# Kernel optimization log

Hardware: AMD Instinct MI355X
Metric: run time of the kernel (lower is better)

## Reference

```python
import jax, jax.numpy as jnp
import numpy as np

B, S, K, N = 2, 4096, 4096, 4096
BLOCKSIZE = 128  # GPTQ group size


def _unpack_rows(q):
    # int32 [K//8, N] -> int32 [K, N], 8 nibbles packed along dim 0 (little-endian)
    shifts = (jnp.arange(8, dtype=jnp.int32) * 4)
    nib = (q[:, None, :] >> shifts[None, :, None]) & 0xF  # [K//8, 8, N]
    return nib.reshape(q.shape[0] * 8, q.shape[1])


def _unpack_cols(q):
    # int32 [G, N//8] -> int32 [G, N], 8 nibbles packed along dim 1
    shifts = (jnp.arange(8, dtype=jnp.int32) * 4)
    nib = (q[:, :, None] >> shifts[None, None, :]) & 0xF  # [G, N//8, 8]
    return nib.reshape(q.shape[0], q.shape[1] * 8)


def _dequant(qweight, scales, qzeros, blocksize):
    # GPTQ int4 dequant: w[k, n] = (q[k, n] - z[g, n]) * s[g, n], g = k // blocksize
    w_int = _unpack_rows(qweight).astype(jnp.float32)          # [K, N]
    zeros = _unpack_cols(qzeros).astype(jnp.float32)           # [G, N]
    z = jnp.repeat(zeros, blocksize, axis=0)                   # [K, N]
    s = jnp.repeat(scales, blocksize, axis=0)                  # [K, N]
    return (w_int - z) * s


def setup_inputs() -> dict:
    key = jax.random.key(0)
    ks = jax.random.split(key, 6)
    inp = jax.random.normal(ks[0], (B, S, K), dtype=jnp.float32)
    residual = jax.random.normal(ks[1], (B, S, N), dtype=jnp.float32)
    qweight = jax.random.randint(ks[2], (K // 8, N), 0, 2147483647, dtype=jnp.int32)
    qzeros = jax.random.randint(ks[3], (K // BLOCKSIZE, N // 8), 0, 2147483647, dtype=jnp.int32)
    scales = jax.random.uniform(ks[4], (K // BLOCKSIZE, N), dtype=jnp.float32, minval=1e-3, maxval=1e-2)
    bias = jax.random.normal(ks[5], (N,), dtype=jnp.float32)
    return {"input": inp, "residual": residual, "qweight": qweight,
            "scales": scales, "qzeros": qzeros, "bias": bias}


def reference(input, residual, qweight, scales, qzeros, bias):
    # Fused: dequant(int4 GPTQ) -> GEMM -> +bias -> +residual (mm_bias_add_int4)
    w = _dequant(qweight, scales, qzeros, BLOCKSIZE)           # [K, N]
    out = jnp.einsum('bsk,kn->bsn', input, w) + bias + residual
    return out
```

## Files before the change

### kernel.cpp

```cpp
#include <hip/hip_runtime.h>
#include <hip/hip_bf16.h>
#include <stdint.h>

using bf16 = __hip_bfloat16;
typedef __attribute__((ext_vector_type(8))) short short8;
typedef __attribute__((ext_vector_type(4))) float floatx4;

#define DEVINL __device__ __forceinline__

constexpr int K_DIM = 4096;
constexpr int N_DIM = 4096;
constexpr int M_DIM = 8192;

DEVINL void gload_lds16(const void* g, void* l) {
  __builtin_amdgcn_global_load_lds((const __attribute__((address_space(1))) void*)g,
                                   (__attribute__((address_space(3))) void*)l,
                                   16, 0, 0);
}

__global__ __launch_bounds__(256) void k_prep(const int* __restrict__ qw,
                                              const float* __restrict__ scales,
                                              const int* __restrict__ qz,
                                              bf16* __restrict__ wt,
                                              const float* __restrict__ a,
                                              bf16* __restrict__ ao) {
  if (blockIdx.x < 64 * 128) {
    __shared__ __align__(16) uint4 lds[32 * 8];
    const int b = blockIdx.x;
    const int kp0 = (b & 63) * 8;
    const int n0  = (b >> 6) * 32;
    const int t = threadIdx.x;
    const int n_l = t & 31, kp_l = t >> 5;
    const int n = n0 + n_l, kp = kp0 + kp_l;

    int q = qw[kp * N_DIM + n];
    int g = kp0 >> 4;
    float s = scales[g * N_DIM + n];
    int zword = qz[g * (N_DIM / 8) + (n >> 3)];
    float z = (float)((zword >> ((n & 7) * 4)) & 0xF);
    float nzs = -z * s;
    bf16 h[8];
#pragma unroll
    for (int i = 0; i < 8; ++i) {
      float w = fmaf((float)((q >> (4 * i)) & 0xF), s, nzs);
      h[i] = __float2bfloat16(w);
    }
    lds[n_l * 8 + (kp_l ^ (n_l & 7))] = *(const uint4*)h;
    __syncthreads();
    const int n_o = t >> 3, kp_o = t & 7;
    uint4 v = lds[n_o * 8 + (kp_o ^ (n_o & 7))];
    ((uint4*)wt)[(size_t)(n0 + n_o) * (K_DIM / 8) + kp0 + kp_o] = v;
  } else {
    int t = (blockIdx.x - 64 * 128) * 256 + threadIdx.x;
    const float4* a4 = (const float4*)a;
    float4 v0 = a4[2 * t], v1 = a4[2 * t + 1];
    bf16 h[8];
    h[0] = __float2bfloat16(v0.x); h[1] = __float2bfloat16(v0.y);
    h[2] = __float2bfloat16(v0.z); h[3] = __float2bfloat16(v0.w);
    h[4] = __float2bfloat16(v1.x); h[5] = __float2bfloat16(v1.y);
    h[6] = __float2bfloat16(v1.z); h[7] = __float2bfloat16(v1.w);
    ((uint4*)ao)[t] = *(const uint4*)h;
  }
}

constexpr int BM = 128, BN = 128, BK = 64;
constexpr int NBLK_N = N_DIM / BN;
constexpr int NBLK_M = M_DIM / BM;

template <bool A_IS_BF16>
__global__ __launch_bounds__(256, 2) void k_gemm(const void* __restrict__ a_ptr,
                                                 const bf16* __restrict__ wt,
                                                 const float* __restrict__ bias,
                                                 const float* __restrict__ residual,
                                                 float* __restrict__ out) {
  __shared__ __align__(16) bf16 As[BM * BK];
  __shared__ __align__(16) bf16 Bs[BN * BK];

  const int tid  = threadIdx.x;
  const int lane = tid & 63;
  const int wave = tid >> 6;
  const int wr = wave >> 1, wc = wave & 1;
  const int quad = lane >> 4, lq = lane & 15;

  const int xcd = blockIdx.x & 7;
  const int idx = blockIdx.x >> 3;
  const int bn = xcd * 4 + (idx & 3);
  const int bm = idx >> 2;
  const int m0 = bm * BM, n0 = bn * BN;

  floatx4 acc[4][4] = {};

  const int st_r8 = lane >> 3;
  const int st_ce = ((lane & 7) ^ (st_r8 & 7)) * 8;
  const int rd_x = lq & 7;

  const bf16*  a_bf = (const bf16*)a_ptr;
  const float* a_f  = (const float*)a_ptr;

  for (int k0 = 0; k0 < K_DIM; k0 += BK) {
    __syncthreads();
#pragma unroll
    for (int j = 0; j < 4; ++j) {
      int g = wave + j * 4;
      const bf16* gp = wt + (size_t)(n0 + g * 8 + st_r8) * K_DIM + k0 + st_ce;
      gload_lds16(gp, &Bs[g * 512]);
    }
    if (A_IS_BF16) {
#pragma unroll
      for (int j = 0; j < 4; ++j) {
        int g = wave + j * 4;
        const bf16* gp = a_bf + (size_t)(m0 + g * 8 + st_r8) * K_DIM + k0 + st_ce;
        gload_lds16(gp, &As[g * 512]);
      }
    } else {
      int row = tid >> 1, half = tid & 1;
      int rx = row & 7;
      const float* srcf = a_f + (size_t)(m0 + row) * K_DIM + k0 + half * 32;
#pragma unroll
      for (int cc = 0; cc < 4; ++cc) {
        int logc = half * 4 + cc;
        float4 v0 = ((const float4*)srcf)[cc * 2];
        float4 v1 = ((const float4*)srcf)[cc * 2 + 1];
        bf16 h[8];
        h[0] = __float2bfloat16(v0.x); h[1] = __float2bfloat16(v0.y);
        h[2] = __float2bfloat16(v0.z); h[3] = __float2bfloat16(v0.w);
        h[4] = __float2bfloat16(v1.x); h[5] = __float2bfloat16(v1.y);
        h[6] = __float2bfloat16(v1.z); h[7] = __float2bfloat16(v1.w);
        *(uint4*)&As[row * BK + ((logc ^ rx) * 8)] = *(const uint4*)h;
      }
    }
    __syncthreads();

#pragma unroll
    for (int s = 0; s < 2; ++s) {
      short8 afr[4], bfr[4];
#pragma unroll
      for (int mi = 0; mi < 4; ++mi)
        afr[mi] = *(const short8*)&As[(wr * 64 + mi * 16 + lq) * BK +
                                      (((s * 4 + quad) ^ rd_x) * 8)];
#pragma unroll
      for (int ni = 0; ni < 4; ++ni)
        bfr[ni] = *(const short8*)&Bs[(wc * 64 + ni * 16 + lq) * BK +
                                      (((s * 4 + quad) ^ rd_x) * 8)];
#pragma unroll
      for (int mi = 0; mi < 4; ++mi)
#pragma unroll
        for (int ni = 0; ni < 4; ++ni)
          acc[mi][ni] = __builtin_amdgcn_mfma_f32_16x16x32_bf16(afr[mi], bfr[ni],
                                                                acc[mi][ni], 0, 0, 0);
    }
  }

#pragma unroll
  for (int ni = 0; ni < 4; ++ni) {
    int col = n0 + wc * 64 + ni * 16 + lq;
    float bv = bias[col];
#pragma unroll
    for (int mi = 0; mi < 4; ++mi) {
      int rbase = m0 + wr * 64 + mi * 16 + quad * 4;
#pragma unroll
      for (int r = 0; r < 4; ++r) {
        size_t idxo = (size_t)(rbase + r) * N_DIM + col;
        out[idxo] = acc[mi][ni][r] + bv + residual[idxo];
      }
    }
  }
}

constexpr int TBK = 64;
constexpr int TNT = K_DIM / TBK;

#define VM4 asm volatile("s_waitcnt vmcnt(4)" ::: "memory")
#define VM0 asm volatile("s_waitcnt vmcnt(0)" ::: "memory")
#define VMN

#define STAGE_A(buf, half, kt) {                                                   \
    const bf16* g0_ = A + (size_t)(m0 + (half) * 128 + wave * 16 + st_r) * K_DIM   \
                        + (kt) * TBK + st_c;                                       \
    gload_lds16(g0_,             &As[buf][(half) * 128 + wave * 16    ][0]);       \
    gload_lds16(g0_ + 8 * K_DIM, &As[buf][(half) * 128 + wave * 16 + 8][0]);       \
  }

#define STAGE_B(buf, half, kt) {                                                   \
    const bf16* g1_ = Bw + (size_t)(n0 + (half) * 128 + wave * 16 + st_r) * K_DIM  \
                        + (kt) * TBK + st_c;                                       \
    gload_lds16(g1_,             &Bs[buf][(half) * 128 + wave * 16    ][0]);       \
    gload_lds16(g1_ + 8 * K_DIM, &Bs[buf][(half) * 128 + wave * 16 + 8][0]);       \
  }

#define PHASE(cur, qm, qn, STG)                                                    \
  {                                                                                \
    short8 afr[4][2], bfr[2][2];                                                   \
    _Pragma("unroll") for (int mi = 0; mi < 4; ++mi) {                             \
      _Pragma("unroll") for (int s = 0; s < 2; ++s)                                \
        afr[mi][s] = *(const short8*)&As[cur][(qm) * 128 + wm * 64 + mi * 16 + l15]\
                                        [rdc[s]];                                  \
    }                                                                              \
    _Pragma("unroll") for (int ni = 0; ni < 2; ++ni) {                             \
      _Pragma("unroll") for (int s = 0; s < 2; ++s)                                \
        bfr[ni][s] = *(const short8*)&Bs[cur][(qn) * 128 + wn * 32 + ni * 16 + l15]\
                                        [rdc[s]];                                  \
    }                                                                              \
    STG;                                                                           \
    __builtin_amdgcn_sched_barrier(0);                                             \
    __builtin_amdgcn_s_barrier();                                                  \
    __builtin_amdgcn_s_setprio(1);                                                 \
    _Pragma("unroll") for (int mi = 0; mi < 4; ++mi) {                             \
      _Pragma("unroll") for (int ni = 0; ni < 2; ++ni) {                           \
        acc[qm][qn][mi][ni] = __builtin_amdgcn_mfma_f32_16x16x32_bf16(             \
            afr[mi][0], bfr[ni][0], acc[qm][qn][mi][ni], 0, 0, 0);                 \
        acc[qm][qn][mi][ni] = __builtin_amdgcn_mfma_f32_16x16x32_bf16(             \
            afr[mi][1], bfr[ni][1], acc[qm][qn][mi][ni], 0, 0, 0);                 \
      }                                                                            \
    }                                                                              \
    __builtin_amdgcn_s_setprio(0);                                                 \
    __builtin_amdgcn_sched_barrier(0);                                             \
  }

#define TILE(cur, SHI, SLO, thi, tlo, VMW)                                         \
  PHASE(cur, 0, 0, if (SHI) STAGE_A((cur) ^ 1, 1, thi))                            \
  __builtin_amdgcn_s_barrier();                                                    \
  PHASE(cur, 0, 1, if (SHI) STAGE_B((cur) ^ 1, 1, thi))                            \
  __builtin_amdgcn_s_barrier();                                                    \
  PHASE(cur, 1, 0, if (SLO) STAGE_A((cur), 0, tlo))                                \
  __builtin_amdgcn_s_barrier();                                                    \
  PHASE(cur, 1, 1, if (SLO) STAGE_B((cur), 0, tlo))                                \
  VMW;                                                                             \
  __builtin_amdgcn_s_barrier();

__global__ __launch_bounds__(512, 2) void k_gemm8(const bf16* __restrict__ A,
                                                  const bf16* __restrict__ Bw,
                                                  const float* __restrict__ bias,
                                                  const float* __restrict__ residual,
                                                  float* __restrict__ out) {
  __shared__ __align__(16) bf16 As[2][256][TBK];
  __shared__ __align__(16) bf16 Bs[2][256][TBK];

  const int tid  = threadIdx.x;
  const int lane = tid & 63;
  const int wave = tid >> 6;
  const int wm = wave >> 2;
  const int wn = wave & 3;
  const int quad = lane >> 4, l15 = lane & 15;

  const int wgid = (blockIdx.x & 7) * 64 + (blockIdx.x >> 3);
  const int bn = (wgid >> 6) * 2 + (wgid & 1);
  const int bm = (wgid & 63) >> 1;
  const int m0 = bm * 256, n0 = bn * 256;

  const int st_r = lane >> 3;
  const int st_c = ((lane & 7) ^ st_r) * 8;

  const int rdc[2] = { ((quad)     ^ (l15 & 7)) * 8,
                       ((4 + quad) ^ (l15 & 7)) * 8 };

  floatx4 acc[2][2][4][2] = {};

  STAGE_A(0, 0, 0)
  STAGE_B(0, 0, 0)
  STAGE_A(0, 1, 0)
  STAGE_B(0, 1, 0)
  STAGE_A(1, 0, 1)
  STAGE_B(1, 0, 1)
  VM4;
  __builtin_amdgcn_s_barrier();

#pragma unroll 1
  for (int t = 0; t < TNT - 2; t += 2) {
    TILE(0, true, true, t + 1, t + 2, VM4)
    TILE(1, true, true, t + 2, t + 3, VM4)
  }
  TILE(0, true, false, TNT - 1, 0, VM0)
  TILE(1, false, false, 0, 0, VMN)

#pragma unroll
  for (int qn = 0; qn < 2; ++qn)
#pragma unroll
    for (int ni = 0; ni < 2; ++ni) {
      int col = n0 + qn * 128 + wn * 32 + ni * 16 + l15;
      float bv = bias[col];
#pragma unroll
      for (int qm = 0; qm < 2; ++qm)
#pragma unroll
        for (int mi = 0; mi < 4; ++mi) {
          int rbase = m0 + qm * 128 + wm * 64 + mi * 16 + quad * 4;
#pragma unroll
          for (int r = 0; r < 4; ++r) {
            size_t o = (size_t)(rbase + r) * N_DIM + col;
            out[o] = acc[qm][qn][mi][ni][r] + bv + residual[o];
          }
        }
    }
}

extern "C" void kernel_launch(void* const* d_in, const int* in_sizes, int n_in,
                              void* d_out, int out_size, void* d_ws, size_t ws_size,
                              hipStream_t stream) {
  const float* input    = (const float*)d_in[0];
  const float* residual = (const float*)d_in[1];
  const int*   qweight  = (const int*)d_in[2];
  const float* scales   = (const float*)d_in[3];
  const int*   qzeros   = (const int*)d_in[4];
  const float* bias     = (const float*)d_in[5];
  float* out = (float*)d_out;

  const size_t wt_bytes = (size_t)N_DIM * K_DIM * sizeof(bf16);
  const size_t a_bytes  = (size_t)M_DIM * K_DIM * sizeof(bf16);

  bf16* wt = (bf16*)d_ws;

  if (ws_size >= wt_bytes + a_bytes) {
    bf16* a_bf = (bf16*)((char*)d_ws + wt_bytes);
    k_prep<<<64 * 128 + (M_DIM * K_DIM / 8) / 256, 256, 0, stream>>>(
        qweight, scales, qzeros, wt, input, a_bf);
    k_gemm8<<<(M_DIM / 256) * (N_DIM / 256), 512, 0, stream>>>(
        a_bf, wt, bias, residual, out);
  } else {
    k_prep<<<64 * 128, 256, 0, stream>>>(qweight, scales, qzeros, wt, input, nullptr);
    k_gemm<false><<<NBLK_M * NBLK_N, 256, 0, stream>>>(input, wt, bias, residual, out);
  }
}
```

Measured before the change: 645.9 us.

## Restructure GEMM main loop into two half-phases with B fragments reused

Replaces the four-phase-per-tile schedule (each phase reloading A and B fragments and hitting a barrier) with a two-phase schedule. All B fragments for the tile are loaded once and reused across both M halves. Staging of the next tile is issued early into the other buffer, with vmcnt waits retuned to 6 and 2. Global pointers are now advanced incrementally instead of being recomputed. This cuts LDS reads and barriers per tile, at the cost of more live registers for B fragments and a different overlap of loads and waits.

Result: faster. 598.2 us (-7.4%).

```diff
diff --git a/kernel.cpp b/kernel.cpp
--- a/kernel.cpp
+++ b/kernel.cpp
@@ -170,63 +170,74 @@
 constexpr int TBK = 64;
 constexpr int TNT = K_DIM / TBK;
 
-#define VM4 asm volatile("s_waitcnt vmcnt(4)" ::: "memory")
-#define VM0 asm volatile("s_waitcnt vmcnt(0)" ::: "memory")
-#define VMN
-
-#define STAGE_A(buf, half, kt) {                                                   \
-    const bf16* g0_ = A + (size_t)(m0 + (half) * 128 + wave * 16 + st_r) * K_DIM   \
-                        + (kt) * TBK + st_c;                                       \
-    gload_lds16(g0_,             &As[buf][(half) * 128 + wave * 16    ][0]);       \
-    gload_lds16(g0_ + 8 * K_DIM, &As[buf][(half) * 128 + wave * 16 + 8][0]);       \
-  }
-
-#define STAGE_B(buf, half, kt) {                                                   \
-    const bf16* g1_ = Bw + (size_t)(n0 + (half) * 128 + wave * 16 + st_r) * K_DIM  \
-                        + (kt) * TBK + st_c;                                       \
-    gload_lds16(g1_,             &Bs[buf][(half) * 128 + wave * 16    ][0]);       \
-    gload_lds16(g1_ + 8 * K_DIM, &Bs[buf][(half) * 128 + wave * 16 + 8][0]);       \
-  }
-
-#define PHASE(cur, qm, qn, STG)                                                    \
+#define SB0  __builtin_amdgcn_sched_barrier(0)
+#define SBAR __builtin_amdgcn_s_barrier()
+#define VMW(n) asm volatile("s_waitcnt vmcnt(" #n ")" ::: "memory")
+
+#define STAGE_A(buf, half, p) {                                                    \
+    gload_lds16((p) + (size_t)(half) * 128 * K_DIM,                                \
+                &As[buf][(half) * 128 + wave * 16][0]);                            \
+    gload_lds16((p) + (size_t)(half) * 128 * K_DIM + 8 * K_DIM,                    \
+                &As[buf][(half) * 128 + wave * 16 + 8][0]);                        \
+  }
+
+#define STAGE_B(buf, half, p) {                                                    \
+    gload_lds16((p) + (size_t)(half) * 128 * K_DIM,                                \
+                &Bs[buf][(half) * 128 + wave * 16][0]);                            \
+    gload_lds16((p) + (size_t)(half) * 128 * K_DIM + 8 * K_DIM,                    \
+                &Bs[buf][(half) * 128 + wave * 16 + 8][0]);                        \
+  }
+
+#define TILE(c, DO_STAGE, LAST)                                                    \
   {                                                                                \
-    short8 afr[4][2], bfr[2][2];                                                   \
-    _Pragma("unroll") for (int mi = 0; mi < 4; ++mi) {                             \
+                                        \
+    short8 bfr[2][2][2], a0[4][2];                                                 \
+    _Pragma("unroll") for (int qn = 0; qn < 2; ++qn)                               \
+      _Pragma("unroll") for (int ni = 0; ni < 2; ++ni)                             \
+        _Pragma("unroll") for (int s = 0; s < 2; ++s)                              \
+          bfr[qn][ni][s] = *(const short8*)                                        \
+              &Bs[c][qn * 128 + wn * 32 + ni * 16 + l15][rdc[s]];                  \
+    _Pragma("unroll") for (int mi = 0; mi < 4; ++mi)                               \
       _Pragma("unroll") for (int s = 0; s < 2; ++s)                                \
-        afr[mi][s] = *(const short8*)&As[cur][(qm) * 128 + wm * 64 + mi * 16 + l15]\
-                                        [rdc[s]];                                  \
+        a0[mi][s] = *(const short8*)&As[c][wm * 64 + mi * 16 + l15][rdc[s]];       \
+    if (DO_STAGE) {                                                                \
+      STAGE_A((c) ^ 1, 0, aP)                                                      \
+      STAGE_B((c) ^ 1, 0, bP)                                                      \
+      STAGE_B((c) ^ 1, 1, bP)                                                      \
     }                                                                              \
-    _Pragma("unroll") for (int ni = 0; ni < 2; ++ni) {                             \
+    SB0;                                                                           \
+    __builtin_amdgcn_s_setprio(1);                                                 \
+    _Pragma("unroll") for (int s = 0; s < 2; ++s)                                  \
+      _Pragma("unroll") for (int mi = 0; mi < 4; ++mi)                             \
+        _Pragma("unroll") for (int qn = 0; qn < 2; ++qn)                           \
+          _Pragma("unroll") for (int ni = 0; ni < 2; ++ni)                         \
+            acc[0][qn][mi][ni] = __builtin_amdgcn_mfma_f32_16x16x32_bf16(          \
+                a0[mi][s], bfr[qn][ni][s], acc[0][qn][mi][ni], 0, 0, 0);           \
+    __builtin_amdgcn_s_setprio(0);                                                 \
+    SB0;                                                                           \
+    if (LAST) { VMW(0); } else { VMW(6); }                                         \
+    SBAR;                                                                          \
+                                        \
+    short8 a1[4][2];                                                               \
+    _Pragma("unroll") for (int mi = 0; mi < 4; ++mi)                               \
       _Pragma("unroll") for (int s = 0; s < 2; ++s)                                \
-        bfr[ni][s] = *(const short8*)&Bs[cur][(qn) * 128 + wn * 32 + ni * 16 + l15]\
-                                        [rdc[s]];                                  \
+        a1[mi][s] = *(const short8*)&As[c][128 + wm * 64 + mi * 16 + l15][rdc[s]]; \
+    if (DO_STAGE) {                                                                \
+      STAGE_A((c) ^ 1, 1, aP)                                                      \
+      aP += TBK; bP += TBK;                                                        \
     }                                                                              \
-    STG;                                                                           \
-    __builtin_amdgcn_sched_barrier(0);                                             \
-    __builtin_amdgcn_s_barrier();                                                  \
+    SB0;                                                                           \
     __builtin_amdgcn_s_setprio(1);                                                 \
-    _Pragma("unroll") for (int mi = 0; mi < 4; ++mi) {                             \
-      _Pragma("unroll") for (int ni = 0; ni < 2; ++ni) {                           \
-        acc[qm][qn][mi][ni] = __builtin_amdgcn_mfma_f32_16x16x32_bf16(             \
-            afr[mi][0], bfr[ni][0], acc[qm][qn][mi][ni], 0, 0, 0);                 \
-        acc[qm][qn][mi][ni] = __builtin_amdgcn_mfma_f32_16x16x32_bf16(             \
-            afr[mi][1], bfr[ni][1], acc[qm][qn][mi][ni], 0, 0, 0);                 \
-      }                                                                            \
-    }                                                                              \
+    _Pragma("unroll") for (int s = 0; s < 2; ++s)                                  \
+      _Pragma("unroll") for (int mi = 0; mi < 4; ++mi)                             \
+        _Pragma("unroll") for (int qn = 0; qn < 2; ++qn)                           \
+          _Pragma("unroll") for (int ni = 0; ni < 2; ++ni)                         \
+            acc[1][qn][mi][ni] = __builtin_amdgcn_mfma_f32_16x16x32_bf16(          \
+                a1[mi][s], bfr[qn][ni][s], acc[1][qn][mi][ni], 0, 0, 0);           \
     __builtin_amdgcn_s_setprio(0);                                                 \
-    __builtin_amdgcn_sched_barrier(0);                                             \
-  }
-
-#define TILE(cur, SHI, SLO, thi, tlo, VMW)                                         \
-  PHASE(cur, 0, 0, if (SHI) STAGE_A((cur) ^ 1, 1, thi))                            \
-  __builtin_amdgcn_s_barrier();                                                    \
-  PHASE(cur, 0, 1, if (SHI) STAGE_B((cur) ^ 1, 1, thi))                            \
-  __builtin_amdgcn_s_barrier();                                                    \
-  PHASE(cur, 1, 0, if (SLO) STAGE_A((cur), 0, tlo))                                \
-  __builtin_amdgcn_s_barrier();                                                    \
-  PHASE(cur, 1, 1, if (SLO) STAGE_B((cur), 0, tlo))                                \
-  VMW;                                                                             \
-  __builtin_amdgcn_s_barrier();
+    SB0;                                                                           \
+    if (!LAST) { VMW(2); SBAR; }                                                   \
+  }
 
 __global__ __launch_bounds__(512, 2) void k_gemm8(const bf16* __restrict__ A,
                                                   const bf16* __restrict__ Bw,
@@ -256,22 +267,24 @@
 
   floatx4 acc[2][2][4][2] = {};
 
-  STAGE_A(0, 0, 0)
-  STAGE_B(0, 0, 0)
-  STAGE_A(0, 1, 0)
-  STAGE_B(0, 1, 0)
-  STAGE_A(1, 0, 1)
-  STAGE_B(1, 0, 1)
-  VM4;
-  __builtin_amdgcn_s_barrier();
+  const bf16* aP = A  + (size_t)(m0 + wave * 16 + st_r) * K_DIM + st_c;
+  const bf16* bP = Bw + (size_t)(n0 + wave * 16 + st_r) * K_DIM + st_c;
+
+  STAGE_A(0, 0, aP)
+  STAGE_B(0, 0, bP)
+  STAGE_B(0, 1, bP)
+  STAGE_A(0, 1, aP)
+  aP += TBK; bP += TBK;
+  VMW(2);
+  SBAR;
 
 #pragma unroll 1
   for (int t = 0; t < TNT - 2; t += 2) {
-    TILE(0, true, true, t + 1, t + 2, VM4)
-    TILE(1, true, true, t + 2, t + 3, VM4)
-  }
-  TILE(0, true, false, TNT - 1, 0, VM0)
-  TILE(1, false, false, 0, 0, VMN)
+    TILE(0, true, false)
+    TILE(1, true, false)
+  }
+  TILE(0, true, false)
+  TILE(1, false, true)
 
 #pragma unroll
   for (int qn = 0; qn < 2; ++qn)
```
